# Kernel tuning notes

Measured on AMD Instinct MI355X. Metric: run time of the kernel, lower is better.

The kernel has to match this reference:

```python
import jax, jax.numpy as jnp
import numpy as np

B, S, D = 16, 2048, 128


def setup_inputs() -> dict:
    key = jax.random.key(0)
    kq, kk, kv = jax.random.split(key, 3)
    return {
        "queries": jax.random.normal(kq, (B, S, D), dtype=jnp.float32),
        "keys": jax.random.normal(kk, (B, S, D), dtype=jnp.float32),
        "values": jax.random.normal(kv, (B, S, D), dtype=jnp.float32),
        "mask": jnp.zeros((B, S, S), dtype=bool),  # True -> masked out
    }


def reference(queries, keys, values, mask):
    d_k = queries.shape[-1]
    scale = 1.0 / np.sqrt(d_k).astype(np.float32)
    # scores: [B, S, S]
    scores = jnp.einsum("bqd,bkd->bqk", queries, keys) * scale
    scores = jnp.where(mask, -jnp.inf, scores)
    attn_weights = jax.nn.softmax(scores, axis=-1)
    # dropout prob = 0.0 (eval), identity
    output = jnp.einsum("bqk,bkd->bqd", attn_weights, values)
    return output
```

## Files before the change

### kernel.cpp

```cpp
#include <hip/hip_runtime.h>
#include <hip/hip_bf16.h>

#define SEQ    2048
#define DIM    128
#define NBATCH 16
#define KVB    32
#define NSPLIT 4
#define QUART  (SEQ / NSPLIT)
#define NTILE  (QUART / KVB)
#define QW     32
#define NWAVE  4
#define QB     (QW * NWAVE)
#define NROW   (NBATCH * SEQ)
#define TELEM  (KVB * DIM)

typedef __bf16 bf16x8 __attribute__((ext_vector_type(8)));
typedef float  f32x4  __attribute__((ext_vector_type(4)));
typedef unsigned int uint;

#define LOG2E  1.44269504088896340736f
#define NEGINF (-__builtin_inff())

#define CVT_PK(d, lo, hi) asm("v_cvt_pk_bf16_f32 %0, %1, %2" : "=v"(d) : "v"(lo), "v"(hi))
#define SWAP32(x, y) asm("v_permlane32_swap_b32 %0, %1" : "+v"(x), "+v"(y))
#define SWAP16(x, y) asm("v_permlane16_swap_b32 %0, %1" : "+v"(x), "+v"(y))

typedef const __attribute__((address_space(1))) uint* gup;
typedef       __attribute__((address_space(3))) uint* lup;
#define GLDS16(g, l) __builtin_amdgcn_global_load_lds((gup)(g), (lup)(l), 16, 0, 0)

#define APPLY_MASK(mw, s)                          \
    if (mw) {                                      \
        if (mw & 0x000000ffu) s[0] = NEGINF;       \
        if (mw & 0x0000ff00u) s[1] = NEGINF;       \
        if (mw & 0x00ff0000u) s[2] = NEGINF;       \
        if (mw & 0xff000000u) s[3] = NEGINF;       \
    }

__global__ __launch_bounds__(256)
void sdpa_prep(const float* __restrict__ Kg, const float* __restrict__ Vg,
               __bf16* __restrict__ Kb, __bf16* __restrict__ Vb)
{
    const int tile = (int)blockIdx.x;
    const int tid  = (int)threadIdx.x;
    const size_t row0 = (size_t)tile * KVB;

    {
        const int kr = tid >> 3;
        const int c2 = (tid & 7) * 2;
        const int kx = kr & 7;
        const float* src = Kg + (row0 + kr) * DIM;
        __bf16* dst = Kb + (size_t)tile * TELEM + (size_t)kr * DIM;
        #pragma unroll
        for (int c = 0; c < 2; ++c) {
            const int ci = c2 + c;
            const int sc = ci ^ kx;
            const float4 a = *(const float4*)(src + sc * 8);
            const float4 b = *(const float4*)(src + sc * 8 + 4);
            bf16x8 h;
            h[0]=(__bf16)a.x; h[1]=(__bf16)a.y; h[2]=(__bf16)a.z; h[3]=(__bf16)a.w;
            h[4]=(__bf16)b.x; h[5]=(__bf16)b.y; h[6]=(__bf16)b.z; h[7]=(__bf16)b.w;
            *(bf16x8*)(dst + ci * 8) = h;
        }
    }
    {
        const int vd = tid & 127;
        const int cp = (tid >> 7) * 2;
        const int vx = (vd >> 1) & 3;
        const float* src = Vg + row0 * DIM + vd;
        __bf16* dst = Vb + (size_t)tile * TELEM + (size_t)vd * KVB;
        #pragma unroll
        for (int c = 0; c < 2; ++c) {
            const int ck = cp + c;
            const int ci = ck ^ vx;
            bf16x8 h;
            #pragma unroll
            for (int j = 0; j < 8; ++j) h[j] = (__bf16)src[(size_t)(ck * 8 + j) * DIM];
            *(bf16x8*)(dst + ci * 8) = h;
        }
    }
}

__global__ __launch_bounds__(256, 3)
void sdpa_main(const float* __restrict__ Qg, const __bf16* __restrict__ Kbf,
               const __bf16* __restrict__ Vbf, const unsigned char* __restrict__ Mg,
               float* __restrict__ Uw, float* __restrict__ Lw)
{
    __shared__ __bf16 Ksh[2][TELEM];
    __shared__ __bf16 Vsh[2][TELEM];

    const int tid  = (int)threadIdx.x;
    const int wid  = tid >> 6;
    const int lane = tid & 63;
    const int lg   = lane >> 4;
    const int lr   = lane & 15;

    const int bid  = (int)blockIdx.x;
    const int nbid = (bid & 7) * 128 + (bid >> 3);
    const int qtl  = nbid & 15;
    const int g    = nbid >> 4;
    const int quar = g & 3;
    const int bb   = g >> 2;
    const int q0w  = qtl * QB + wid * QW;

    const float qscale = 0.08838834764831845f * LOG2E;

    bf16x8 aqA[4], aqB[4];
    #pragma unroll
    for (int gq = 0; gq < 2; ++gq) {
        const float* qrow = Qg + ((size_t)(bb * SEQ + q0w + gq * 16 + lr)) * DIM;
        #pragma unroll
        for (int kb = 0; kb < 4; ++kb) {
            const float4 f0 = *(const float4*)(qrow + kb * 32 + lg * 8);
            const float4 f1 = *(const float4*)(qrow + kb * 32 + lg * 8 + 4);
            bf16x8 h;
            h[0] = (__bf16)(f0.x * qscale); h[1] = (__bf16)(f0.y * qscale);
            h[2] = (__bf16)(f0.z * qscale); h[3] = (__bf16)(f0.w * qscale);
            h[4] = (__bf16)(f1.x * qscale); h[5] = (__bf16)(f1.y * qscale);
            h[6] = (__bf16)(f1.z * qscale); h[7] = (__bf16)(f1.w * qscale);
            if (gq == 0) aqA[kb] = h; else aqB[kb] = h;
        }
    }

    const __bf16* Kt0 = Kbf + (size_t)(bb * 64 + quar * 16) * TELEM;
    const __bf16* Vt0 = Vbf + (size_t)(bb * 64 + quar * 16) * TELEM;
    const unsigned char* MrowA = Mg + (size_t)bb * SEQ * SEQ
                               + (size_t)(q0w + lr) * SEQ + quar * QUART;
    const unsigned char* MrowB = MrowA + (size_t)16 * SEQ;

    uint mA0, mA1, mB0, mB1;
    const int loff = lane * 16;

    auto issue = [&](int t, int b) {
        const char* Ks = (const char*)(Kt0 + (size_t)t * TELEM);
        const char* Vs = (const char*)(Vt0 + (size_t)t * TELEM);
        char* Kd = (char*)Ksh[b];
        char* Vd = (char*)Vsh[b];
        #pragma unroll
        for (int j = 0; j < 2; ++j) {
            const int o = wid * 1024 + j * 4096;
            GLDS16(Ks + o + loff, Kd + o);
            GLDS16(Vs + o + loff, Vd + o);
        }
        const unsigned char* msA = MrowA + t * KVB + lg * 4;
        mA0 = *(const uint*)(msA);
        mA1 = *(const uint*)(msA + 16);
        const unsigned char* msB = MrowB + t * KVB + lg * 4;
        mB0 = *(const uint*)(msB);
        mB1 = *(const uint*)(msB + 16);
    };

    issue(0, 0);

    f32x4 accA[8], accB[8];
    #pragma unroll
    for (int i = 0; i < 8; ++i) { accA[i] = (f32x4)(0.0f); accB[i] = (f32x4)(0.0f); }
    float lA = 0.0f, lB = 0.0f;

    const int kxr = lr & 7;
    const int vxr = (lr >> 1) & 3;

    for (int t = 0; t < NTILE; ++t) {
        asm volatile("s_waitcnt vmcnt(0)" ::: "memory");
        __syncthreads();
        const uint wA0 = mA0, wA1 = mA1, wB0 = mB0, wB1 = mB1;
        if (t + 1 < NTILE) issue(t + 1, (t + 1) & 1);

        const bf16x8* const Kc = (const bf16x8*)Ksh[t & 1];
        const bf16x8* const Vc = (const bf16x8*)Vsh[t & 1];

        f32x4 sA0 = (f32x4)(0.0f), sA1 = (f32x4)(0.0f);
        f32x4 sB0 = (f32x4)(0.0f), sB1 = (f32x4)(0.0f);
        __builtin_amdgcn_s_setprio(1);
        #pragma unroll
        for (int kb = 0; kb < 4; ++kb) {
            const int ch = (kb * 4 + lg) ^ kxr;
            const bf16x8 a0 = Kc[(lr)      * 16 + ch];
            const bf16x8 a1 = Kc[(16 + lr) * 16 + ch];
            sA0 = __builtin_amdgcn_mfma_f32_16x16x32_bf16(a0, aqA[kb], sA0, 0, 0, 0);
            sB0 = __builtin_amdgcn_mfma_f32_16x16x32_bf16(a0, aqB[kb], sB0, 0, 0, 0);
            sA1 = __builtin_amdgcn_mfma_f32_16x16x32_bf16(a1, aqA[kb], sA1, 0, 0, 0);
            sB1 = __builtin_amdgcn_mfma_f32_16x16x32_bf16(a1, aqB[kb], sB1, 0, 0, 0);
        }
        __builtin_amdgcn_s_setprio(0);

        APPLY_MASK(wA0, sA0) APPLY_MASK(wA1, sA1)
        APPLY_MASK(wB0, sB0) APPLY_MASK(wB1, sB1)

        float psA = 0.0f, psB = 0.0f;
        #pragma unroll
        for (int r = 0; r < 4; ++r) { sA0[r] = __builtin_amdgcn_exp2f(sA0[r]); psA += sA0[r]; }
        #pragma unroll
        for (int r = 0; r < 4; ++r) { sA1[r] = __builtin_amdgcn_exp2f(sA1[r]); psA += sA1[r]; }
        #pragma unroll
        for (int r = 0; r < 4; ++r) { sB0[r] = __builtin_amdgcn_exp2f(sB0[r]); psB += sB0[r]; }
        #pragma unroll
        for (int r = 0; r < 4; ++r) { sB1[r] = __builtin_amdgcn_exp2f(sB1[r]); psB += sB1[r]; }
        lA += psA;
        lB += psB;

        bf16x8 apA, apB;
        {
            uint a0w, a1w, b0w, b1w;
            CVT_PK(a0w, sA0[0], sA0[1]); CVT_PK(a1w, sA0[2], sA0[3]);
            CVT_PK(b0w, sA1[0], sA1[1]); CVT_PK(b1w, sA1[2], sA1[3]);
            SWAP32(a0w, b0w); SWAP16(a0w, b0w);
            SWAP32(a1w, b1w); SWAP16(a1w, b1w);
            union W { uint w[4]; bf16x8 v; } u;
            u.w[0] = a0w; u.w[1] = a1w; u.w[2] = b0w; u.w[3] = b1w;
            apA = u.v;
        }
        {
            uint a0w, a1w, b0w, b1w;
            CVT_PK(a0w, sB0[0], sB0[1]); CVT_PK(a1w, sB0[2], sB0[3]);
            CVT_PK(b0w, sB1[0], sB1[1]); CVT_PK(b1w, sB1[2], sB1[3]);
            SWAP32(a0w, b0w); SWAP16(a0w, b0w);
            SWAP32(a1w, b1w); SWAP16(a1w, b1w);
            union W { uint w[4]; bf16x8 v; } u;
            u.w[0] = a0w; u.w[1] = a1w; u.w[2] = b0w; u.w[3] = b1w;
            apB = u.v;
        }

        __builtin_amdgcn_s_setprio(1);
        #pragma unroll
        for (int nt = 0; nt < 8; ++nt) {
            const bf16x8 bv = Vc[(nt * 16 + lr) * 4 + (lg ^ vxr)];
            accA[nt] = __builtin_amdgcn_mfma_f32_16x16x32_bf16(apA, bv, accA[nt], 0, 0, 0);
            accB[nt] = __builtin_amdgcn_mfma_f32_16x16x32_bf16(apB, bv, accB[nt], 0, 0, 0);
        }
        __builtin_amdgcn_s_setprio(0);
    }

    lA += __shfl_xor(lA, 16); lA += __shfl_xor(lA, 32);
    lB += __shfl_xor(lB, 16); lB += __shfl_xor(lB, 32);
    if (lg == 0) {
        Lw[(size_t)quar * NROW + bb * SEQ + q0w + lr]      = lA;
        Lw[(size_t)quar * NROW + bb * SEQ + q0w + 16 + lr] = lB;
    }

    float* ubA = Uw + ((size_t)quar * NROW + bb * SEQ + q0w + lg * 4) * DIM + lr;
    float* ubB = ubA + (size_t)16 * DIM;
    #pragma unroll
    for (int r = 0; r < 4; ++r)
        #pragma unroll
        for (int nt = 0; nt < 8; ++nt) {
            ubA[(size_t)r * DIM + nt * 16] = accA[nt][r];
            ubB[(size_t)r * DIM + nt * 16] = accB[nt][r];
        }
}

__global__ __launch_bounds__(256)
void sdpa_combine(float* __restrict__ Og, const float* __restrict__ Uw,
                  const float* __restrict__ Lw)
{
    const int gid = (int)blockIdx.x * 256 + (int)threadIdx.x;
    const int row = gid >> 5;
    const float inv = 1.0f / (Lw[row] + Lw[NROW + row]
                            + Lw[2 * NROW + row] + Lw[3 * (size_t)NROW + row]);
    const size_t slab = (size_t)NROW * DIM / 4;
    const float4* U = (const float4*)Uw;
    const float4 a = U[gid];
    const float4 b = U[slab + gid];
    const float4 c = U[2 * slab + gid];
    const float4 d = U[3 * slab + gid];
    float4 o;
    o.x = (a.x + b.x + c.x + d.x) * inv;
    o.y = (a.y + b.y + c.y + d.y) * inv;
    o.z = (a.z + b.z + c.z + d.z) * inv;
    o.w = (a.w + b.w + c.w + d.w) * inv;
    ((float4*)Og)[gid] = o;
}

extern "C" void kernel_launch(void* const* d_in, const int* in_sizes, int n_in,
                              void* d_out, int out_size, void* d_ws, size_t ws_size,
                              hipStream_t stream) {
    const float* Q = (const float*)d_in[0];
    const float* K = (const float*)d_in[1];
    const float* V = (const float*)d_in[2];
    const unsigned char* M = (const unsigned char*)d_in[3];
    float* O  = (float*)d_out;
    float*  Uw  = (float*)d_ws;
    float*  Lw  = Uw + (size_t)NSPLIT * NROW * DIM;
    __bf16* Kbf = (__bf16*)(Lw + (size_t)NSPLIT * NROW);
    __bf16* Vbf = Kbf + (size_t)NROW * DIM;
    sdpa_prep<<<dim3(NROW / KVB), dim3(256), 0, stream>>>(K, V, Kbf, Vbf);
    sdpa_main<<<dim3(NBATCH * 16 * NSPLIT), dim3(256), 0, stream>>>(Q, Kbf, Vbf, M, Uw, Lw);
    sdpa_combine<<<dim3(NROW * DIM / 4 / 256), dim3(256), 0, stream>>>(O, Uw, Lw);
}
```

Baseline: 91.88 us.

## Switch attention main loop from 16x16x32 to 32x32x16 MFMA tiles

Replaces the paired 16x16x32 bf16 MFMAs with 32x32x16 MFMAs for both QK^T and PV. Each wave now handles its 32 query rows as one 32x32 tile. The mask, exp and permlane repacking, LDS addressing, row-sum reduction and output store are reworked for the 32x32 accumulator layout. The aim is fewer MFMA issues and fewer LDS fragment loads per tile, at the cost of a different register layout and dependent MFMA chains.

```diff
diff --git a/kernel.cpp b/kernel.cpp
--- a/kernel.cpp
+++ b/kernel.cpp
@@ -15,7 +15,7 @@
 #define TELEM  (KVB * DIM)
 
 typedef __bf16 bf16x8 __attribute__((ext_vector_type(8)));
-typedef float  f32x4  __attribute__((ext_vector_type(4)));
+typedef float  f32x16 __attribute__((ext_vector_type(16)));
 typedef unsigned int uint;
 
 #define LOG2E  1.44269504088896340736f
@@ -23,19 +23,10 @@
 
 #define CVT_PK(d, lo, hi) asm("v_cvt_pk_bf16_f32 %0, %1, %2" : "=v"(d) : "v"(lo), "v"(hi))
 #define SWAP32(x, y) asm("v_permlane32_swap_b32 %0, %1" : "+v"(x), "+v"(y))
-#define SWAP16(x, y) asm("v_permlane16_swap_b32 %0, %1" : "+v"(x), "+v"(y))
 
 typedef const __attribute__((address_space(1))) uint* gup;
 typedef       __attribute__((address_space(3))) uint* lup;
 #define GLDS16(g, l) __builtin_amdgcn_global_load_lds((gup)(g), (lup)(l), 16, 0, 0)
-
-#define APPLY_MASK(mw, s)                          \
-    if (mw) {                                      \
-        if (mw & 0x000000ffu) s[0] = NEGINF;       \
-        if (mw & 0x0000ff00u) s[1] = NEGINF;       \
-        if (mw & 0x00ff0000u) s[2] = NEGINF;       \
-        if (mw & 0xff000000u) s[3] = NEGINF;       \
-    }
 
 __global__ __launch_bounds__(256)
 void sdpa_prep(const float* __restrict__ Kg, const float* __restrict__ Vg,
@@ -92,8 +83,10 @@
     const int tid  = (int)threadIdx.x;
     const int wid  = tid >> 6;
     const int lane = tid & 63;
-    const int lg   = lane >> 4;
-    const int lr   = lane & 15;
+    const int l31  = lane & 31;
+    const int hi   = lane >> 5;
+    const int kx7  = l31 & 7;
+    const int vx3  = (l31 >> 1) & 3;
 
     const int bid  = (int)blockIdx.x;
     const int nbid = (bid & 7) * 128 + (bid >> 3);
@@ -105,30 +98,28 @@
 
     const float qscale = 0.08838834764831845f * LOG2E;
 
-    bf16x8 aqA[4], aqB[4];
-    #pragma unroll
-    for (int gq = 0; gq < 2; ++gq) {
-        const float* qrow = Qg + ((size_t)(bb * SEQ + q0w + gq * 16 + lr)) * DIM;
-        #pragma unroll
-        for (int kb = 0; kb < 4; ++kb) {
-            const float4 f0 = *(const float4*)(qrow + kb * 32 + lg * 8);
-            const float4 f1 = *(const float4*)(qrow + kb * 32 + lg * 8 + 4);
+    bf16x8 aq[8];
+    {
+        const float* qrow = Qg + ((size_t)(bb * SEQ + q0w + l31)) * DIM;
+        #pragma unroll
+        for (int m = 0; m < 8; ++m) {
+            const float4 f0 = *(const float4*)(qrow + m * 16 + hi * 8);
+            const float4 f1 = *(const float4*)(qrow + m * 16 + hi * 8 + 4);
             bf16x8 h;
             h[0] = (__bf16)(f0.x * qscale); h[1] = (__bf16)(f0.y * qscale);
             h[2] = (__bf16)(f0.z * qscale); h[3] = (__bf16)(f0.w * qscale);
             h[4] = (__bf16)(f1.x * qscale); h[5] = (__bf16)(f1.y * qscale);
             h[6] = (__bf16)(f1.z * qscale); h[7] = (__bf16)(f1.w * qscale);
-            if (gq == 0) aqA[kb] = h; else aqB[kb] = h;
+            aq[m] = h;
         }
     }
 
     const __bf16* Kt0 = Kbf + (size_t)(bb * 64 + quar * 16) * TELEM;
     const __bf16* Vt0 = Vbf + (size_t)(bb * 64 + quar * 16) * TELEM;
-    const unsigned char* MrowA = Mg + (size_t)bb * SEQ * SEQ
-                               + (size_t)(q0w + lr) * SEQ + quar * QUART;
-    const unsigned char* MrowB = MrowA + (size_t)16 * SEQ;
-
-    uint mA0, mA1, mB0, mB1;
+    const unsigned char* Mrow = Mg + (size_t)bb * SEQ * SEQ
+                              + (size_t)(q0w + l31) * SEQ + quar * QUART + 4 * hi;
+
+    uint mn0, mn1, mn2, mn3;
     const int loff = lane * 16;
 
     auto issue = [&](int t, int b) {
@@ -142,111 +133,105 @@
             GLDS16(Ks + o + loff, Kd + o);
             GLDS16(Vs + o + loff, Vd + o);
         }
-        const unsigned char* msA = MrowA + t * KVB + lg * 4;
-        mA0 = *(const uint*)(msA);
-        mA1 = *(const uint*)(msA + 16);
-        const unsigned char* msB = MrowB + t * KVB + lg * 4;
-        mB0 = *(const uint*)(msB);
-        mB1 = *(const uint*)(msB + 16);
+        const unsigned char* ms = Mrow + t * KVB;
+        mn0 = *(const uint*)(ms);
+        mn1 = *(const uint*)(ms + 8);
+        mn2 = *(const uint*)(ms + 16);
+        mn3 = *(const uint*)(ms + 24);
     };
 
     issue(0, 0);
 
-    f32x4 accA[8], accB[8];
+    f32x16 acc[4];
     #pragma unroll
-    for (int i = 0; i < 8; ++i) { accA[i] = (f32x4)(0.0f); accB[i] = (f32x4)(0.0f); }
-    float lA = 0.0f, lB = 0.0f;
-
-    const int kxr = lr & 7;
-    const int vxr = (lr >> 1) & 3;
+    for (int i = 0; i < 4; ++i) acc[i] = (f32x16)(0.0f);
+    float l_run = 0.0f;
 
     for (int t = 0; t < NTILE; ++t) {
         asm volatile("s_waitcnt vmcnt(0)" ::: "memory");
         __syncthreads();
-        const uint wA0 = mA0, wA1 = mA1, wB0 = mB0, wB1 = mB1;
+        const uint mw0 = mn0, mw1 = mn1, mw2 = mn2, mw3 = mn3;
         if (t + 1 < NTILE) issue(t + 1, (t + 1) & 1);
 
         const bf16x8* const Kc = (const bf16x8*)Ksh[t & 1];
         const bf16x8* const Vc = (const bf16x8*)Vsh[t & 1];
 
-        f32x4 sA0 = (f32x4)(0.0f), sA1 = (f32x4)(0.0f);
-        f32x4 sB0 = (f32x4)(0.0f), sB1 = (f32x4)(0.0f);
+        f32x16 s = (f32x16)(0.0f);
         __builtin_amdgcn_s_setprio(1);
         #pragma unroll
-        for (int kb = 0; kb < 4; ++kb) {
-            const int ch = (kb * 4 + lg) ^ kxr;
-            const bf16x8 a0 = Kc[(lr)      * 16 + ch];
-            const bf16x8 a1 = Kc[(16 + lr) * 16 + ch];
-            sA0 = __builtin_amdgcn_mfma_f32_16x16x32_bf16(a0, aqA[kb], sA0, 0, 0, 0);
-            sB0 = __builtin_amdgcn_mfma_f32_16x16x32_bf16(a0, aqB[kb], sB0, 0, 0, 0);
-            sA1 = __builtin_amdgcn_mfma_f32_16x16x32_bf16(a1, aqA[kb], sA1, 0, 0, 0);
-            sB1 = __builtin_amdgcn_mfma_f32_16x16x32_bf16(a1, aqB[kb], sB1, 0, 0, 0);
+        for (int m = 0; m < 8; ++m) {
+            const bf16x8 a = Kc[l31 * 16 + ((2 * m + hi) ^ kx7)];
+            s = __builtin_amdgcn_mfma_f32_32x32x16_bf16(a, aq[m], s, 0, 0, 0);
         }
         __builtin_amdgcn_s_setprio(0);
 
-        APPLY_MASK(wA0, sA0) APPLY_MASK(wA1, sA1)
-        APPLY_MASK(wB0, sB0) APPLY_MASK(wB1, sB1)
-
-        float psA = 0.0f, psB = 0.0f;
-        #pragma unroll
-        for (int r = 0; r < 4; ++r) { sA0[r] = __builtin_amdgcn_exp2f(sA0[r]); psA += sA0[r]; }
-        #pragma unroll
-        for (int r = 0; r < 4; ++r) { sA1[r] = __builtin_amdgcn_exp2f(sA1[r]); psA += sA1[r]; }
-        #pragma unroll
-        for (int r = 0; r < 4; ++r) { sB0[r] = __builtin_amdgcn_exp2f(sB0[r]); psB += sB0[r]; }
-        #pragma unroll
-        for (int r = 0; r < 4; ++r) { sB1[r] = __builtin_amdgcn_exp2f(sB1[r]); psB += sB1[r]; }
-        lA += psA;
-        lB += psB;
-
-        bf16x8 apA, apB;
-        {
-            uint a0w, a1w, b0w, b1w;
-            CVT_PK(a0w, sA0[0], sA0[1]); CVT_PK(a1w, sA0[2], sA0[3]);
-            CVT_PK(b0w, sA1[0], sA1[1]); CVT_PK(b1w, sA1[2], sA1[3]);
-            SWAP32(a0w, b0w); SWAP16(a0w, b0w);
-            SWAP32(a1w, b1w); SWAP16(a1w, b1w);
-            union W { uint w[4]; bf16x8 v; } u;
-            u.w[0] = a0w; u.w[1] = a1w; u.w[2] = b0w; u.w[3] = b1w;
-            apA = u.v;
-        }
-        {
-            uint a0w, a1w, b0w, b1w;
-            CVT_PK(a0w, sB0[0], sB0[1]); CVT_PK(a1w, sB0[2], sB0[3]);
-            CVT_PK(b0w, sB1[0], sB1[1]); CVT_PK(b1w, sB1[2], sB1[3]);
-            SWAP32(a0w, b0w); SWAP16(a0w, b0w);
-            SWAP32(a1w, b1w); SWAP16(a1w, b1w);
-            union W { uint w[4]; bf16x8 v; } u;
-            u.w[0] = a0w; u.w[1] = a1w; u.w[2] = b0w; u.w[3] = b1w;
-            apB = u.v;
-        }
+        if (mw0) {
+            if (mw0 & 0x000000ffu) s[0] = NEGINF;
+            if (mw0 & 0x0000ff00u) s[1] = NEGINF;
+            if (mw0 & 0x00ff0000u) s[2] = NEGINF;
+            if (mw0 & 0xff000000u) s[3] = NEGINF;
+        }
+        if (mw1) {
+            if (mw1 & 0x000000ffu) s[4] = NEGINF;
+            if (mw1 & 0x0000ff00u) s[5] = NEGINF;
+            if (mw1 & 0x00ff0000u) s[6] = NEGINF;
+            if (mw1 & 0xff000000u) s[7] = NEGINF;
+        }
+        if (mw2) {
+            if (mw2 & 0x000000ffu) s[8]  = NEGINF;
+            if (mw2 & 0x0000ff00u) s[9]  = NEGINF;
+            if (mw2 & 0x00ff0000u) s[10] = NEGINF;
+            if (mw2 & 0xff000000u) s[11] = NEGINF;
+        }
+        if (mw3) {
+            if (mw3 & 0x000000ffu) s[12] = NEGINF;
+            if (mw3 & 0x0000ff00u) s[13] = NEGINF;
+            if (mw3 & 0x00ff0000u) s[14] = NEGINF;
+            if (mw3 & 0xff000000u) s[15] = NEGINF;
+        }
+
+        float ps = 0.0f;
+        #pragma unroll
+        for (int r = 0; r < 16; ++r) { s[r] = __builtin_amdgcn_exp2f(s[r]); ps += s[r]; }
+        l_run += ps;
+
+        uint w0, w1, w2, w3, w4, w5, w6, w7;
+        CVT_PK(w0, s[0],  s[1]);  CVT_PK(w1, s[2],  s[3]);
+        CVT_PK(w2, s[4],  s[5]);  CVT_PK(w3, s[6],  s[7]);
+        CVT_PK(w4, s[8],  s[9]);  CVT_PK(w5, s[10], s[11]);
+        CVT_PK(w6, s[12], s[13]); CVT_PK(w7, s[14], s[15]);
+        SWAP32(w0, w2); SWAP32(w1, w3);
+        SWAP32(w4, w6); SWAP32(w5, w7);
+        union W { uint w[4]; bf16x8 v; } u0, u1;
+        u0.w[0] = w0; u0.w[1] = w1; u0.w[2] = w2; u0.w[3] = w3;
+        u1.w[0] = w4; u1.w[1] = w5; u1.w[2] = w6; u1.w[3] = w7;
+        const bf16x8 pa0 = u0.v;
+        const bf16x8 pa1 = u1.v;
 
         __builtin_amdgcn_s_setprio(1);
         #pragma unroll
-        for (int nt = 0; nt < 8; ++nt) {
-            const bf16x8 bv = Vc[(nt * 16 + lr) * 4 + (lg ^ vxr)];
-            accA[nt] = __builtin_amdgcn_mfma_f32_16x16x32_bf16(apA, bv, accA[nt], 0, 0, 0);
-            accB[nt] = __builtin_amdgcn_mfma_f32_16x16x32_bf16(apB, bv, accB[nt], 0, 0, 0);
+        for (int c = 0; c < 4; ++c) {
+            const int dd = (c * 32 + l31) * 4;
+            const bf16x8 bv0 = Vc[dd + (hi ^ vx3)];
+            acc[c] = __builtin_amdgcn_mfma_f32_32x32x16_bf16(pa0, bv0, acc[c], 0, 0, 0);
+            const bf16x8 bv1 = Vc[dd + ((2 + hi) ^ vx3)];
+            acc[c] = __builtin_amdgcn_mfma_f32_32x32x16_bf16(pa1, bv1, acc[c], 0, 0, 0);
         }
         __builtin_amdgcn_s_setprio(0);
     }
 
-    lA += __shfl_xor(lA, 16); lA += __shfl_xor(lA, 32);
-    lB += __shfl_xor(lB, 16); lB += __shfl_xor(lB, 32);
-    if (lg == 0) {
-        Lw[(size_t)quar * NROW + bb * SEQ + q0w + lr]      = lA;
-        Lw[(size_t)quar * NROW + bb * SEQ + q0w + 16 + lr] = lB;
-    }
-
-    float* ubA = Uw + ((size_t)quar * NROW + bb * SEQ + q0w + lg * 4) * DIM + lr;
-    float* ubB = ubA + (size_t)16 * DIM;
+    l_run += __shfl_xor(l_run, 32);
+    if (hi == 0)
+        Lw[(size_t)quar * NROW + bb * SEQ + q0w + l31] = l_run;
+
+    float* ub = Uw + ((size_t)quar * NROW + bb * SEQ + q0w) * DIM + l31;
     #pragma unroll
-    for (int r = 0; r < 4; ++r)
-        #pragma unroll
-        for (int nt = 0; nt < 8; ++nt) {
-            ubA[(size_t)r * DIM + nt * 16] = accA[nt][r];
-            ubB[(size_t)r * DIM + nt * 16] = accB[nt][r];
-        }
+    for (int r = 0; r < 16; ++r) {
+        const int q = (r & 3) + 8 * (r >> 2) + 4 * hi;
+        #pragma unroll
+        for (int c = 0; c < 4; ++c)
+            ub[(size_t)q * DIM + c * 32] = acc[c][r];
+    }
 }
 
 __global__ __launch_bounds__(256)
```

Result: no change. 92.37 us (+0.5%).
